# Performance work log

Hardware: AMD Instinct MI355X
Metric: run time of the kernel (lower is better)

Reference implementation:

```python
import jax, jax.numpy as jnp
import numpy as np

H, C = 4, 32  # heads, per-head channels (hidden_channels)
N_NODES = 50000


def _transformer_conv(x, src, dst, ea, Wq, bq, Wk, bk, Wv, bv, We, Ws, bs):
    """PyG TransformerConv: concat heads, root weight, edge_dim attention."""
    N = x.shape[0]
    q = (x @ Wq + bq).reshape(N, H, C)
    k = (x @ Wk + bk).reshape(N, H, C)
    v = (x @ Wv + bv).reshape(N, H, C)
    e = (ea @ We).reshape(-1, H, C)                      # [E,H,C]
    k_e = k[src] + e                                     # gather + edge bias
    alpha = jnp.sum(q[dst] * k_e, axis=-1) / jnp.sqrt(jnp.float32(C))  # [E,H]
    # segment softmax over incoming edges of each dst node
    m = jax.ops.segment_max(alpha, dst, num_segments=N)  # [N,H]
    alpha = jnp.exp(alpha - m[dst])
    denom = jax.ops.segment_sum(alpha, dst, num_segments=N)[dst]
    alpha = alpha / (denom + 1e-16)
    msg = alpha[..., None] * (v[src] + e)                # [E,H,C]
    out = jax.ops.segment_sum(msg, dst, num_segments=N).reshape(N, H * C)
    return out + x @ Ws + bs                             # skip (root weight)


def setup_inputs() -> dict:
    key = jax.random.key(0)
    ks = jax.random.split(key, 20)
    E = 400000
    d = H * C  # 128
    s = 0.05
    return {
        "x": jax.random.normal(ks[0], (N_NODES, d), jnp.float32),
        "edge_index": jax.random.randint(ks[1], (2, E), 0, N_NODES, jnp.int32),
        "edge_attr": jax.random.normal(ks[2], (E, 2), jnp.float32),
        "Wq": jax.random.normal(ks[3], (3, d, d), jnp.float32) * s,
        "bq": jax.random.normal(ks[4], (3, d), jnp.float32) * s,
        "Wk": jax.random.normal(ks[5], (3, d, d), jnp.float32) * s,
        "bk": jax.random.normal(ks[6], (3, d), jnp.float32) * s,
        "Wv": jax.random.normal(ks[7], (3, d, d), jnp.float32) * s,
        "bv": jax.random.normal(ks[8], (3, d), jnp.float32) * s,
        "We": jax.random.normal(ks[9], (3, 2, d), jnp.float32) * s,
        "Ws": jax.random.normal(ks[10], (3, d, d), jnp.float32) * s,
        "bs": jax.random.normal(ks[11], (3, d), jnp.float32) * s,
        "W1": jax.random.normal(ks[12], (d, C), jnp.float32) * s,
        "b1": jax.random.normal(ks[13], (C,), jnp.float32) * s,
        "W2": jax.random.normal(ks[14], (C, 8), jnp.float32) * s,
        "b2": jax.random.normal(ks[15], (8,), jnp.float32) * s,
    }


def reference(x, edge_index, edge_attr, Wq, bq, Wk, bk, Wv, bv, We, Ws, bs, W1, b1, W2, b2):
    src, dst = edge_index[0], edge_index[1]
    h = x
    for l in range(3):  # three TransformerConv layers (dropout is identity in eval)
        h = jax.nn.leaky_relu(
            _transformer_conv(h, src, dst, edge_attr,
                              Wq[l], bq[l], Wk[l], bk[l], Wv[l], bv[l],
                              We[l], Ws[l], bs[l]),
            negative_slope=0.01)
    emb = jax.nn.leaky_relu(h @ W1 + b1, negative_slope=0.01)
    logits = emb @ W2 + b2
    return jax.nn.log_softmax(logits, axis=1)
```

## Files before the change

### kernel.cpp

```cpp
#include <hip/hip_runtime.h>
#include <hip/hip_bf16.h>
#include <math.h>

#define HD 128
#define NH 4
#define CC 32

typedef __attribute__((ext_vector_type(8))) short short8;
typedef __attribute__((ext_vector_type(4))) float f32x4;

__device__ __forceinline__ float leaky(float x) { return x > 0.f ? x : 0.01f * x; }

__device__ __forceinline__ ushort bf16_rne(float f) {
    unsigned u = __float_as_uint(f);
    return (ushort)((u + 0x7fffu + ((u >> 16) & 1u)) >> 16);
}
__device__ __forceinline__ float bf16_f(ushort h) {
    return __uint_as_float(((unsigned)h) << 16);
}

#define WFRAG_HALF (12 * 32 * 64 * 8)

__global__ __launch_bounds__(256) void conv_w(
    const float* __restrict__ Wq, const float* __restrict__ Wk,
    const float* __restrict__ Wv, const float* __restrict__ Wsk,
    ushort* __restrict__ frag)
{
    int tid = blockIdx.x * 256 + threadIdx.x;
    if (tid >= 12 * 8 * 4 * 64) return;
    int lane = tid & 63;
    int kk = (tid >> 6) & 3;
    int ct = (tid >> 8) & 7;
    int mg = tid >> 11;
    int l = mg >> 2, m = mg & 3;
    const float* src = ((m == 0) ? Wq : (m == 1) ? Wk : (m == 2) ? Wv : Wsk)
                       + (size_t)l * HD * HD;
    int col = ct * 16 + (lane & 15);
    int k0 = kk * 32 + (lane >> 4) * 8;
    ushort* dst = frag + (size_t)tid * 8;
#pragma unroll
    for (int j = 0; j < 8; ++j) {
        float w = src[(size_t)(k0 + j) * HD + col];
        ushort h = bf16_rne(w);
        dst[j] = h;
        dst[WFRAG_HALF + j] = bf16_rne(w - bf16_f(h));
    }
}

__global__ __launch_bounds__(512) void gemm4_mfma(
    const float* __restrict__ X, const ushort* __restrict__ Wfrag,
    const float* __restrict__ bq, const float* __restrict__ bk,
    const float* __restrict__ bv, const float* __restrict__ bsk,
    float* __restrict__ Oq, float* __restrict__ Ok,
    float* __restrict__ Ov, float* __restrict__ Osk,
    int layer, int N)
{
    __shared__ __align__(16) ushort Xh[64 * HD];
    __shared__ __align__(16) ushort Xl[64 * HD];
    __shared__ __align__(16) float  Ot[8][16 * 36];

    int t = threadIdx.x;
    int row0 = blockIdx.x * 64;

#pragma unroll
    for (int i = 0; i < 4; ++i) {
        int idx = t + i * 512;
        int r = idx >> 5;
        int c4 = (idx & 31) * 4;
        int gr = row0 + r;
        float4 xv = (gr < N) ? *(const float4*)(X + (size_t)gr * HD + c4)
                             : make_float4(0.f, 0.f, 0.f, 0.f);
        ushort h0 = bf16_rne(xv.x), h1 = bf16_rne(xv.y),
               h2 = bf16_rne(xv.z), h3 = bf16_rne(xv.w);
        ushort l0 = bf16_rne(xv.x - bf16_f(h0)), l1 = bf16_rne(xv.y - bf16_f(h1)),
               l2 = bf16_rne(xv.z - bf16_f(h2)), l3 = bf16_rne(xv.w - bf16_f(h3));
        int off = r * 256 + c4 * 2;
        int swz = off ^ ((r & 7) << 4);
        *(ushort4*)((char*)Xh + swz) = make_ushort4(h0, h1, h2, h3);
        *(ushort4*)((char*)Xl + swz) = make_ushort4(l0, l1, l2, l3);
    }
    __syncthreads();

    int w = t >> 6;
    int p = w & 3;
    int h = w >> 2;
    int lane = t & 63;
    int col16 = lane & 15;
    int quad = lane >> 4;
    float* scratch = Ot[w];

#pragma unroll
    for (int mm = 0; mm < 2; ++mm) {
        int mat = blockIdx.y * 2 + mm;
        const float* b = (mat == 0) ? bq : (mat == 1) ? bk : (mat == 2) ? bv : bsk;
        float* O = (mat == 0) ? Oq : (mat == 1) ? Ok : (mat == 2) ? Ov : Osk;
        int mg = layer * 4 + mat;

        short8 bh[2][4], bl[2][4];
#pragma unroll
        for (int cl = 0; cl < 2; ++cl) {
            int ct = p * 2 + cl;
#pragma unroll
            for (int kk = 0; kk < 4; ++kk) {
                const ushort* wp = Wfrag + ((size_t)((mg * 8 + ct) * 4 + kk) * 64 + lane) * 8;
                bh[cl][kk] = *(const short8*)wp;
                bl[cl][kk] = *(const short8*)(wp + WFRAG_HALF);
            }
        }
        float bcol0 = b[(p * 2 + 0) * 16 + col16];
        float bcol1 = b[(p * 2 + 1) * 16 + col16];

#pragma unroll
        for (int mtl = 0; mtl < 2; ++mtl) {
            int arow = h * 32 + mtl * 16 + col16;
            int abase = arow * 256;
            int aswz = (arow & 7) << 4;
            f32x4 c0a = {0.f,0.f,0.f,0.f}, c0b = {0.f,0.f,0.f,0.f}, c0c = {0.f,0.f,0.f,0.f};
            f32x4 c1a = {0.f,0.f,0.f,0.f}, c1b = {0.f,0.f,0.f,0.f}, c1c = {0.f,0.f,0.f,0.f};
#pragma unroll
            for (int kk = 0; kk < 4; ++kk) {
                int koff = abase + kk * 64 + quad * 16;
                short8 ah = *(const short8*)((const char*)Xh + (koff ^ aswz));
                short8 al = *(const short8*)((const char*)Xl + (koff ^ aswz));
                c0a = __builtin_amdgcn_mfma_f32_16x16x32_bf16(ah, bh[0][kk], c0a, 0, 0, 0);
                c0b = __builtin_amdgcn_mfma_f32_16x16x32_bf16(ah, bl[0][kk], c0b, 0, 0, 0);
                c0c = __builtin_amdgcn_mfma_f32_16x16x32_bf16(al, bh[0][kk], c0c, 0, 0, 0);
                c1a = __builtin_amdgcn_mfma_f32_16x16x32_bf16(ah, bh[1][kk], c1a, 0, 0, 0);
                c1b = __builtin_amdgcn_mfma_f32_16x16x32_bf16(ah, bl[1][kk], c1b, 0, 0, 0);
                c1c = __builtin_amdgcn_mfma_f32_16x16x32_bf16(al, bh[1][kk], c1c, 0, 0, 0);
            }
#pragma unroll
            for (int i = 0; i < 4; ++i) {
                int rr = quad * 4 + i;
                scratch[rr * 36 + col16]      = c0a[i] + c0b[i] + c0c[i] + bcol0;
                scratch[rr * 36 + 16 + col16] = c1a[i] + c1b[i] + c1c[i] + bcol1;
            }
#pragma unroll
            for (int s = 0; s < 2; ++s) {
                int row = s * 8 + (lane >> 3);
                int c4 = (lane & 7) * 4;
                float4 v = *(const float4*)(&scratch[row * 36 + c4]);
                int gr = row0 + h * 32 + mtl * 16 + row;
                if (gr < N)
                    *(float4*)(O + (size_t)gr * HD + p * 32 + c4) = v;
            }
        }
    }
}

__global__ __launch_bounds__(256) void count_deg(
    const int* __restrict__ ei, int* __restrict__ deg, int E)
{
    int e = blockIdx.x * 256 + threadIdx.x;
    if (e < E) atomicAdd(&deg[ei[E + e]], 1);
}

__global__ __launch_bounds__(1024) void scan_kernel(
    const int* __restrict__ deg, int* __restrict__ off,
    int* __restrict__ cursor, int N)
{
    __shared__ int wsum[16];
    __shared__ int carry_s;
    int tid = threadIdx.x;
    int lane = tid & 63;
    int w = tid >> 6;
    if (tid == 0) carry_s = 0;
    __syncthreads();
    for (int base = 0; base < N; base += 1024) {
        int idx = base + tid;
        int x = (idx < N) ? deg[idx] : 0;
        int val = x;
#pragma unroll
        for (int s = 1; s < 64; s <<= 1) {
            int t = __shfl_up(val, s);
            if (lane >= s) val += t;
        }
        if (lane == 63) wsum[w] = val;
        __syncthreads();
        if (w == 0) {
            int t = (lane < 16) ? wsum[lane] : 0;
#pragma unroll
            for (int s = 1; s < 16; s <<= 1) {
                int u = __shfl_up(t, s);
                if (lane >= s) t += u;
            }
            if (lane < 16) wsum[lane] = t;
        }
        __syncthreads();
        int carry = carry_s;
        int wexcl = (w > 0) ? wsum[w - 1] : 0;
        int excl = carry + wexcl + (val - x);
        if (idx < N) { off[idx] = excl; cursor[idx] = excl; }
        __syncthreads();
        if (tid == 0) carry_s = carry + wsum[15];
        __syncthreads();
    }
    if (threadIdx.x == 0) off[N] = carry_s;
}

__global__ __launch_bounds__(256) void scatter_edges(
    const int* __restrict__ ei, const float* __restrict__ ea,
    int* __restrict__ cursor, float4* __restrict__ meta, int E)
{
    int e = blockIdx.x * 256 + threadIdx.x;
    if (e >= E) return;
    int dst = ei[E + e];
    int pos = atomicAdd(&cursor[dst], 1);
    meta[pos] = make_float4(__int_as_float(ei[e]), ea[2 * e], ea[2 * e + 1], 0.f);
}

__global__ __launch_bounds__(256) void fused_attn(
    const float* __restrict__ q, const float* __restrict__ k,
    const float* __restrict__ v, const float* __restrict__ skip,
    const int* __restrict__ off, const float4* __restrict__ meta,
    const float* __restrict__ We, float* __restrict__ hout, int N)
{
    int wid = (int)((blockIdx.x * 256 + threadIdx.x) >> 6);
    int lane = threadIdx.x & 63;
    if (wid >= N) return;
    int c = lane * 2;

    float2 w0 = *(const float2*)(We + c);
    float2 w1 = *(const float2*)(We + HD + c);
    float2 q2 = *(const float2*)(q + (size_t)wid * HD + c);

    float m = -INFINITY, s = 0.f;
    float ox = 0.f, oy = 0.f;

    int beg = off[wid], end = off[wid + 1];
    for (int j = beg; j < end; ++j) {
        float4 md = meta[j];
        int src = __float_as_int(md.x);
        float ex = md.y * w0.x + md.z * w1.x;
        float ey = md.y * w0.y + md.z * w1.y;
        float2 kv = *(const float2*)(k + (size_t)src * HD + c);
        float2 vv = *(const float2*)(v + (size_t)src * HD + c);
        float p = q2.x * (kv.x + ex) + q2.y * (kv.y + ey);
        p += __shfl_xor(p, 1);
        p += __shfl_xor(p, 2);
        p += __shfl_xor(p, 4);
        p += __shfl_xor(p, 8);
        p *= 0.17677669529663687f;
        float mn = fmaxf(m, p);
        float scale = __expf(m - mn);
        float pe = __expf(p - mn);
        s = s * scale + pe;
        ox = ox * scale + pe * (vv.x + ex);
        oy = oy * scale + pe * (vv.y + ey);
        m = mn;
    }

    float inv = 1.f / (s + 1e-16f);
    float2 sk = *(const float2*)(skip + (size_t)wid * HD + c);
    float2 hv;
    hv.x = leaky(ox * inv + sk.x);
    hv.y = leaky(oy * inv + sk.y);
    *(float2*)(hout + (size_t)wid * HD + c) = hv;
}

__global__ __launch_bounds__(256) void emb_kernel(
    const float* __restrict__ h, const float* __restrict__ W1,
    const float* __restrict__ b1, float* __restrict__ emb, int N)
{
    int i = blockIdx.x * 256 + threadIdx.x;
    if (i >= N * CC) return;
    int row = i >> 5, col = i & 31;
    const float* hr = h + (size_t)row * HD;
    float acc = 0.f;
#pragma unroll 4
    for (int k = 0; k < HD; ++k) acc += hr[k] * W1[k * CC + col];
    emb[i] = leaky(acc + b1[col]);
}

__global__ __launch_bounds__(256) void logits_kernel(
    const float* __restrict__ emb, const float* __restrict__ W2,
    const float* __restrict__ b2, float* __restrict__ out, int N)
{
    int i = blockIdx.x * 256 + threadIdx.x;
    int row = i >> 3, col = i & 7;
    if (row >= N) return;
    const float* er = emb + (size_t)row * CC;
    float acc = b2[col];
#pragma unroll
    for (int k = 0; k < CC; ++k) acc += er[k] * W2[k * 8 + col];
    float mx = acc;
    mx = fmaxf(mx, __shfl_xor(mx, 1));
    mx = fmaxf(mx, __shfl_xor(mx, 2));
    mx = fmaxf(mx, __shfl_xor(mx, 4));
    float ex = expf(acc - mx);
    float sm = ex;
    sm += __shfl_xor(sm, 1);
    sm += __shfl_xor(sm, 2);
    sm += __shfl_xor(sm, 4);
    out[i] = acc - mx - logf(sm);
}

extern "C" void kernel_launch(void* const* d_in, const int* in_sizes, int n_in,
                              void* d_out, int out_size, void* d_ws, size_t ws_size,
                              hipStream_t stream)
{
    const float* x  = (const float*)d_in[0];
    const int*   ei = (const int*)d_in[1];
    const float* ea = (const float*)d_in[2];
    const float* Wq = (const float*)d_in[3];
    const float* bq = (const float*)d_in[4];
    const float* Wk = (const float*)d_in[5];
    const float* bk = (const float*)d_in[6];
    const float* Wv = (const float*)d_in[7];
    const float* bv = (const float*)d_in[8];
    const float* We = (const float*)d_in[9];
    const float* Ws = (const float*)d_in[10];
    const float* bs = (const float*)d_in[11];
    const float* W1 = (const float*)d_in[12];
    const float* b1 = (const float*)d_in[13];
    const float* W2 = (const float*)d_in[14];
    const float* b2 = (const float*)d_in[15];

    int N = in_sizes[0] / HD;
    int E = in_sizes[1] / 2;

    float* ws = (float*)d_ws;
    size_t nd = (size_t)N * HD;
    float* hbuf = ws;
    float* qbuf = ws + nd;
    float* kbuf = ws + 2 * nd;
    float* vbuf = ws + 3 * nd;
    float* sbuf = ws + 4 * nd;
    float4* meta = (float4*)(ws + 5 * nd);
    int* deg    = (int*)(ws + 5 * nd + 4 * (size_t)E);
    int* off    = deg + N;
    int* cursor = off + N + 1;
    size_t frag_byte = (((5 * nd + 4 * (size_t)E) + (size_t)(3 * N + 1)) * 4 + 15)
                       & ~(size_t)15;
    ushort* Wfrag = (ushort*)((char*)d_ws + frag_byte);

    int gemm_gx = (N + 63) / 64;
    int edge_gx = (E + 255) / 256;
    int attn_gx = (N + 3) / 4;

    hipMemsetAsync(deg, 0, (size_t)N * sizeof(int), stream);
    count_deg<<<edge_gx, 256, 0, stream>>>(ei, deg, E);
    scan_kernel<<<1, 1024, 0, stream>>>(deg, off, cursor, N);
    scatter_edges<<<edge_gx, 256, 0, stream>>>(ei, ea, cursor, meta, E);
    conv_w<<<(12 * 8 * 4 * 64 + 255) / 256, 256, 0, stream>>>(Wq, Wk, Wv, Ws, Wfrag);

    for (int l = 0; l < 3; ++l) {
        const float* cur = (l == 0) ? x : hbuf;
        const float* Wel = We + (size_t)l * 2 * HD;

        gemm4_mfma<<<dim3(gemm_gx, 2), 512, 0, stream>>>(
            cur, Wfrag,
            bq + (size_t)l * HD, bk + (size_t)l * HD,
            bv + (size_t)l * HD, bs + (size_t)l * HD,
            qbuf, kbuf, vbuf, sbuf, l, N);

        fused_attn<<<attn_gx, 256, 0, stream>>>(
            qbuf, kbuf, vbuf, sbuf, off, meta, Wel, hbuf, N);
    }

    emb_kernel<<<(N * CC + 255) / 256, 256, 0, stream>>>(hbuf, W1, b1, kbuf, N);
    logits_kernel<<<(N * 8 + 255) / 256, 256, 0, stream>>>(kbuf, W2, b2, (float*)d_out, N);
}
```

Baseline: 608.9 us.

## Split each node's edges across four wavefront quarters with online-softmax merge

The per-node attention kernel now divides the wavefront into four 16-lane groups. Each group handles every fourth incoming edge and loads 8 channels per lane as float4 vectors, so four edges are in flight at once instead of one. The partial softmax states (max, sum, accumulator) are then merged across groups with cross-lane shuffles. This aims to hide gather latency and raise memory-level parallelism on short edge lists, at the cost of extra registers and a merge step at the end.

```diff
diff --git a/kernel.cpp b/kernel.cpp
--- a/kernel.cpp
+++ b/kernel.cpp
@@ -218,44 +218,112 @@
     int wid = (int)((blockIdx.x * 256 + threadIdx.x) >> 6);
     int lane = threadIdx.x & 63;
     if (wid >= N) return;
-    int c = lane * 2;
-
-    float2 w0 = *(const float2*)(We + c);
-    float2 w1 = *(const float2*)(We + HD + c);
-    float2 q2 = *(const float2*)(q + (size_t)wid * HD + c);
-
-    float m = -INFINITY, s = 0.f;
-    float ox = 0.f, oy = 0.f;
+    int quarter = lane >> 4;
+    int ql = lane & 15;
+    int cA = ql * 4;
+    int cB = 64 + ql * 4;
+
+    float4 w0A = *(const float4*)(We + cA);
+    float4 w1A = *(const float4*)(We + HD + cA);
+    float4 w0B = *(const float4*)(We + cB);
+    float4 w1B = *(const float4*)(We + HD + cB);
+    float4 qA = *(const float4*)(q + (size_t)wid * HD + cA);
+    float4 qB = *(const float4*)(q + (size_t)wid * HD + cB);
+
+    float mA = -1e30f, sA = 0.f, mB = -1e30f, sB = 0.f;
+    float4 oA = make_float4(0.f, 0.f, 0.f, 0.f);
+    float4 oB = make_float4(0.f, 0.f, 0.f, 0.f);
 
     int beg = off[wid], end = off[wid + 1];
-    for (int j = beg; j < end; ++j) {
+    for (int j = beg + quarter; j < end; j += 4) {
         float4 md = meta[j];
         int src = __float_as_int(md.x);
-        float ex = md.y * w0.x + md.z * w1.x;
-        float ey = md.y * w0.y + md.z * w1.y;
-        float2 kv = *(const float2*)(k + (size_t)src * HD + c);
-        float2 vv = *(const float2*)(v + (size_t)src * HD + c);
-        float p = q2.x * (kv.x + ex) + q2.y * (kv.y + ey);
-        p += __shfl_xor(p, 1);
-        p += __shfl_xor(p, 2);
-        p += __shfl_xor(p, 4);
-        p += __shfl_xor(p, 8);
-        p *= 0.17677669529663687f;
-        float mn = fmaxf(m, p);
-        float scale = __expf(m - mn);
-        float pe = __expf(p - mn);
-        s = s * scale + pe;
-        ox = ox * scale + pe * (vv.x + ex);
-        oy = oy * scale + pe * (vv.y + ey);
-        m = mn;
-    }
-
-    float inv = 1.f / (s + 1e-16f);
-    float2 sk = *(const float2*)(skip + (size_t)wid * HD + c);
-    float2 hv;
-    hv.x = leaky(ox * inv + sk.x);
-    hv.y = leaky(oy * inv + sk.y);
-    *(float2*)(hout + (size_t)wid * HD + c) = hv;
+        float4 eA, eB;
+        eA.x = md.y * w0A.x + md.z * w1A.x;
+        eA.y = md.y * w0A.y + md.z * w1A.y;
+        eA.z = md.y * w0A.z + md.z * w1A.z;
+        eA.w = md.y * w0A.w + md.z * w1A.w;
+        eB.x = md.y * w0B.x + md.z * w1B.x;
+        eB.y = md.y * w0B.y + md.z * w1B.y;
+        eB.z = md.y * w0B.z + md.z * w1B.z;
+        eB.w = md.y * w0B.w + md.z * w1B.w;
+        float4 kA = *(const float4*)(k + (size_t)src * HD + cA);
+        float4 kB = *(const float4*)(k + (size_t)src * HD + cB);
+        float4 vA = *(const float4*)(v + (size_t)src * HD + cA);
+        float4 vB = *(const float4*)(v + (size_t)src * HD + cB);
+        float pA = qA.x * (kA.x + eA.x) + qA.y * (kA.y + eA.y)
+                 + qA.z * (kA.z + eA.z) + qA.w * (kA.w + eA.w);
+        float pB = qB.x * (kB.x + eB.x) + qB.y * (kB.y + eB.y)
+                 + qB.z * (kB.z + eB.z) + qB.w * (kB.w + eB.w);
+        pA += __shfl_xor(pA, 1); pA += __shfl_xor(pA, 2); pA += __shfl_xor(pA, 4);
+        pB += __shfl_xor(pB, 1); pB += __shfl_xor(pB, 2); pB += __shfl_xor(pB, 4);
+        pA *= 0.17677669529663687f;
+        pB *= 0.17677669529663687f;
+        float mnA = fmaxf(mA, pA);
+        float scA = __expf(mA - mnA);
+        float peA = __expf(pA - mnA);
+        sA = sA * scA + peA;
+        oA.x = oA.x * scA + peA * (vA.x + eA.x);
+        oA.y = oA.y * scA + peA * (vA.y + eA.y);
+        oA.z = oA.z * scA + peA * (vA.z + eA.z);
+        oA.w = oA.w * scA + peA * (vA.w + eA.w);
+        mA = mnA;
+        float mnB = fmaxf(mB, pB);
+        float scB = __expf(mB - mnB);
+        float peB = __expf(pB - mnB);
+        sB = sB * scB + peB;
+        oB.x = oB.x * scB + peB * (vB.x + eB.x);
+        oB.y = oB.y * scB + peB * (vB.y + eB.y);
+        oB.z = oB.z * scB + peB * (vB.z + eB.z);
+        oB.w = oB.w * scB + peB * (vB.w + eB.w);
+        mB = mnB;
+    }
+
+#pragma unroll
+    for (int d = 16; d <= 32; d <<= 1) {
+        float moA = __shfl_xor(mA, d), soA = __shfl_xor(sA, d);
+        float4 ooA;
+        ooA.x = __shfl_xor(oA.x, d); ooA.y = __shfl_xor(oA.y, d);
+        ooA.z = __shfl_xor(oA.z, d); ooA.w = __shfl_xor(oA.w, d);
+        float mmA = fmaxf(mA, moA);
+        float aA = __expf(mA - mmA), bA = __expf(moA - mmA);
+        sA = sA * aA + soA * bA;
+        oA.x = oA.x * aA + ooA.x * bA;
+        oA.y = oA.y * aA + ooA.y * bA;
+        oA.z = oA.z * aA + ooA.z * bA;
+        oA.w = oA.w * aA + ooA.w * bA;
+        mA = mmA;
+        float moB = __shfl_xor(mB, d), soB = __shfl_xor(sB, d);
+        float4 ooB;
+        ooB.x = __shfl_xor(oB.x, d); ooB.y = __shfl_xor(oB.y, d);
+        ooB.z = __shfl_xor(oB.z, d); ooB.w = __shfl_xor(oB.w, d);
+        float mmB = fmaxf(mB, moB);
+        float aB = __expf(mB - mmB), bB = __expf(moB - mmB);
+        sB = sB * aB + soB * bB;
+        oB.x = oB.x * aB + ooB.x * bB;
+        oB.y = oB.y * aB + ooB.y * bB;
+        oB.z = oB.z * aB + ooB.z * bB;
+        oB.w = oB.w * aB + ooB.w * bB;
+        mB = mmB;
+    }
+
+    if (quarter == 0) {
+        float invA = 1.f / (sA + 1e-16f);
+        float invB = 1.f / (sB + 1e-16f);
+        float4 skA = *(const float4*)(skip + (size_t)wid * HD + cA);
+        float4 skB = *(const float4*)(skip + (size_t)wid * HD + cB);
+        float4 hvA, hvB;
+        hvA.x = leaky(oA.x * invA + skA.x);
+        hvA.y = leaky(oA.y * invA + skA.y);
+        hvA.z = leaky(oA.z * invA + skA.z);
+        hvA.w = leaky(oA.w * invA + skA.w);
+        hvB.x = leaky(oB.x * invB + skB.x);
+        hvB.y = leaky(oB.y * invB + skB.y);
+        hvB.z = leaky(oB.z * invB + skB.z);
+        hvB.w = leaky(oB.w * invB + skB.w);
+        *(float4*)(hout + (size_t)wid * HD + cA) = hvA;
+        *(float4*)(hout + (size_t)wid * HD + cB) = hvB;
+    }
 }
 
 __global__ __launch_bounds__(256) void emb_kernel(
```

Result: faster. 583.8 us (-4.1%).

## Pack K/V to interleaved bf16 and split edges across wave quarters

Applied to the files above, without the earlier changes.

Adds a pack_kv kernel that converts K and V to bf16 and interleaves them per node, so each gathered source row is half the bytes and contiguous. The attention kernel now has each quarter-wave handle every fourth edge with 8 channels per lane, then merges the four partial online-softmax states with shuffles. The aim is to cut gather bandwidth and raise memory-level parallelism across edges. The cost is an extra pack pass per layer and bf16 rounding of K and V.

```diff
diff --git a/kernel.cpp b/kernel.cpp
--- a/kernel.cpp
+++ b/kernel.cpp
@@ -148,6 +148,21 @@
     }
 }
 
+__global__ __launch_bounds__(256) void pack_kv(
+    const float* __restrict__ k, const float* __restrict__ v,
+    ushort* __restrict__ kv, int N)
+{
+    int i = blockIdx.x * 256 + threadIdx.x;
+    if (i >= N * 32) return;
+    int node = i >> 5, g = i & 31;
+    float4 kf = *(const float4*)(k + (size_t)node * HD + g * 4);
+    float4 vf = *(const float4*)(v + (size_t)node * HD + g * 4);
+    ushort4 ku = make_ushort4(bf16_rne(kf.x), bf16_rne(kf.y), bf16_rne(kf.z), bf16_rne(kf.w));
+    ushort4 vu = make_ushort4(bf16_rne(vf.x), bf16_rne(vf.y), bf16_rne(vf.z), bf16_rne(vf.w));
+    *(ushort4*)(kv + (size_t)node * 256 + g * 4) = ku;
+    *(ushort4*)(kv + (size_t)node * 256 + 128 + g * 4) = vu;
+}
+
 __global__ __launch_bounds__(256) void count_deg(
     const int* __restrict__ ei, int* __restrict__ deg, int E)
 {
@@ -210,52 +225,97 @@
 }
 
 __global__ __launch_bounds__(256) void fused_attn(
-    const float* __restrict__ q, const float* __restrict__ k,
-    const float* __restrict__ v, const float* __restrict__ skip,
+    const float* __restrict__ q, const ushort* __restrict__ kv,
+    const float* __restrict__ skip,
     const int* __restrict__ off, const float4* __restrict__ meta,
     const float* __restrict__ We, float* __restrict__ hout, int N)
 {
     int wid = (int)((blockIdx.x * 256 + threadIdx.x) >> 6);
     int lane = threadIdx.x & 63;
     if (wid >= N) return;
-    int c = lane * 2;
-
-    float2 w0 = *(const float2*)(We + c);
-    float2 w1 = *(const float2*)(We + HD + c);
-    float2 q2 = *(const float2*)(q + (size_t)wid * HD + c);
-
-    float m = -INFINITY, s = 0.f;
-    float ox = 0.f, oy = 0.f;
+    int quarter = lane >> 4;
+    int ql = lane & 15;
+    int c8 = ql * 8;
+
+    float4 w0a = *(const float4*)(We + c8);
+    float4 w0b = *(const float4*)(We + c8 + 4);
+    float4 w1a = *(const float4*)(We + HD + c8);
+    float4 w1b = *(const float4*)(We + HD + c8 + 4);
+    float4 qa = *(const float4*)(q + (size_t)wid * HD + c8);
+    float4 qb = *(const float4*)(q + (size_t)wid * HD + c8 + 4);
+
+    float m = -1e30f, s = 0.f;
+    float o[8];
+#pragma unroll
+    for (int i = 0; i < 8; ++i) o[i] = 0.f;
 
     int beg = off[wid], end = off[wid + 1];
-    for (int j = beg; j < end; ++j) {
+    for (int j = beg + quarter; j < end; j += 4) {
         float4 md = meta[j];
         int src = __float_as_int(md.x);
-        float ex = md.y * w0.x + md.z * w1.x;
-        float ey = md.y * w0.y + md.z * w1.y;
-        float2 kv = *(const float2*)(k + (size_t)src * HD + c);
-        float2 vv = *(const float2*)(v + (size_t)src * HD + c);
-        float p = q2.x * (kv.x + ex) + q2.y * (kv.y + ey);
+        float e[8];
+        e[0] = md.y * w0a.x + md.z * w1a.x;
+        e[1] = md.y * w0a.y + md.z * w1a.y;
+        e[2] = md.y * w0a.z + md.z * w1a.z;
+        e[3] = md.y * w0a.w + md.z * w1a.w;
+        e[4] = md.y * w0b.x + md.z * w1b.x;
+        e[5] = md.y * w0b.y + md.z * w1b.y;
+        e[6] = md.y * w0b.z + md.z * w1b.z;
+        e[7] = md.y * w0b.w + md.z * w1b.w;
+        short8 ku = *(const short8*)(kv + (size_t)src * 256 + c8);
+        short8 vu = *(const short8*)(kv + (size_t)src * 256 + 128 + c8);
+        float kf[8], vf[8];
+#pragma unroll
+        for (int i = 0; i < 8; ++i) {
+            kf[i] = __uint_as_float(((unsigned)(ushort)ku[i]) << 16);
+            vf[i] = __uint_as_float(((unsigned)(ushort)vu[i]) << 16);
+        }
+        float p = qa.x * (kf[0] + e[0]) + qa.y * (kf[1] + e[1])
+                + qa.z * (kf[2] + e[2]) + qa.w * (kf[3] + e[3])
+                + qb.x * (kf[4] + e[4]) + qb.y * (kf[5] + e[5])
+                + qb.z * (kf[6] + e[6]) + qb.w * (kf[7] + e[7]);
         p += __shfl_xor(p, 1);
         p += __shfl_xor(p, 2);
-        p += __shfl_xor(p, 4);
-        p += __shfl_xor(p, 8);
         p *= 0.17677669529663687f;
         float mn = fmaxf(m, p);
-        float scale = __expf(m - mn);
+        float sc = __expf(m - mn);
         float pe = __expf(p - mn);
-        s = s * scale + pe;
-        ox = ox * scale + pe * (vv.x + ex);
-        oy = oy * scale + pe * (vv.y + ey);
+        s = s * sc + pe;
+#pragma unroll
+        for (int i = 0; i < 8; ++i) o[i] = o[i] * sc + pe * (vf[i] + e[i]);
         m = mn;
     }
 
-    float inv = 1.f / (s + 1e-16f);
-    float2 sk = *(const float2*)(skip + (size_t)wid * HD + c);
-    float2 hv;
-    hv.x = leaky(ox * inv + sk.x);
-    hv.y = leaky(oy * inv + sk.y);
-    *(float2*)(hout + (size_t)wid * HD + c) = hv;
+#pragma unroll
+    for (int d = 16; d <= 32; d <<= 1) {
+        float mo = __shfl_xor(m, d), so = __shfl_xor(s, d);
+        float oo[8];
+#pragma unroll
+        for (int i = 0; i < 8; ++i) oo[i] = __shfl_xor(o[i], d);
+        float mm = fmaxf(m, mo);
+        float a = __expf(m - mm), b = __expf(mo - mm);
+        s = s * a + so * b;
+#pragma unroll
+        for (int i = 0; i < 8; ++i) o[i] = o[i] * a + oo[i] * b;
+        m = mm;
+    }
+
+    if (quarter == 0) {
+        float inv = 1.f / (s + 1e-16f);
+        float4 ska = *(const float4*)(skip + (size_t)wid * HD + c8);
+        float4 skb = *(const float4*)(skip + (size_t)wid * HD + c8 + 4);
+        float4 ha, hb;
+        ha.x = leaky(o[0] * inv + ska.x);
+        ha.y = leaky(o[1] * inv + ska.y);
+        ha.z = leaky(o[2] * inv + ska.z);
+        ha.w = leaky(o[3] * inv + ska.w);
+        hb.x = leaky(o[4] * inv + skb.x);
+        hb.y = leaky(o[5] * inv + skb.y);
+        hb.z = leaky(o[6] * inv + skb.z);
+        hb.w = leaky(o[7] * inv + skb.w);
+        *(float4*)(hout + (size_t)wid * HD + c8) = ha;
+        *(float4*)(hout + (size_t)wid * HD + c8 + 4) = hb;
+    }
 }
 
 __global__ __launch_bounds__(256) void emb_kernel(
@@ -333,6 +393,7 @@
     size_t frag_byte = (((5 * nd + 4 * (size_t)E) + (size_t)(3 * N + 1)) * 4 + 15)
                        & ~(size_t)15;
     ushort* Wfrag = (ushort*)((char*)d_ws + frag_byte);
+    ushort* kvbuf = Wfrag + 2 * (size_t)WFRAG_HALF;
 
     int gemm_gx = (N + 63) / 64;
     int edge_gx = (E + 255) / 256;
@@ -354,8 +415,10 @@
             bv + (size_t)l * HD, bs + (size_t)l * HD,
             qbuf, kbuf, vbuf, sbuf, l, N);
 
+        pack_kv<<<(N * 32 + 255) / 256, 256, 0, stream>>>(kbuf, vbuf, kvbuf, N);
+
         fused_attn<<<attn_gx, 256, 0, stream>>>(
-            qbuf, kbuf, vbuf, sbuf, off, meta, Wel, hbuf, N);
+            qbuf, kvbuf, sbuf, off, meta, Wel, hbuf, N);
     }
 
     emb_kernel<<<(N * CC + 255) / 256, 256, 0, stream>>>(hbuf, W1, b1, kbuf, N);
```

New measurement: 562.4 us. -7.6%, faster.
